# Optimization experiments

Measured on AMD Instinct MI355X. Metric: run time of the kernel, lower is better.

Reference implementation:

```python
import jax, jax.numpy as jnp
import numpy as np

DIM = 1536
NH = 12
HD = DIM // NH  # 128
B = 1
F, H, W = 8, 16, 16
S = F * H * W  # 2048
EPS = 1e-6
MAX_POS = 1024


def _rmsnorm(x, g):
    # WanRMSNorm: x * rsqrt(mean(x^2, -1) + eps) * weight  (computed in fp32)
    return x * jax.lax.rsqrt(jnp.mean(x * x, axis=-1, keepdims=True) + EPS) * g


def _rope_apply(x, grid_sizes, freqs):
    # x: [B, S, NH, HD]; freqs: [1024, HD//2] angles. Full (level-0) freqs_i path.
    f, h, w = [int(v) for v in np.asarray(grid_sizes[0])]
    c = HD // 2  # 64
    s0 = c - 2 * (c // 3)  # 22 (frame freqs)
    s1 = c // 3            # 21 (height / width freqs)
    p0 = freqs[:f, :s0]
    p1 = freqs[:h, s0:s0 + s1]
    p2 = freqs[:w, s0 + s1:]
    ang = jnp.concatenate([
        jnp.broadcast_to(p0[:, None, None, :], (f, h, w, s0)),
        jnp.broadcast_to(p1[None, :, None, :], (f, h, w, s1)),
        jnp.broadcast_to(p2[None, None, :, :], (f, h, w, s1)),
    ], axis=-1).reshape(f * h * w, 1, c)  # [S, 1, c]
    cos, sin = jnp.cos(ang), jnp.sin(ang)
    xr = x[0].reshape(S, NH, c, 2)  # pairs -> complex rotation
    x0, x1 = xr[..., 0], xr[..., 1]
    out = jnp.stack([x0 * cos - x1 * sin, x0 * sin + x1 * cos], axis=-1)
    return out.reshape(S, NH, HD)[None].astype(jnp.float32)  # [1, S, NH, HD]


def setup_inputs() -> dict:
    key = jax.random.key(0)
    ks = jax.random.split(key, 8)
    sc = 0.02
    return {
        "x": jax.random.normal(ks[0], (B, S, DIM), jnp.float32),
        "freqs": jax.random.uniform(ks[1], (MAX_POS, HD // 2), jnp.float32, 0.0, 2.0 * np.pi),
        "wq": jax.random.normal(ks[2], (DIM, DIM), jnp.float32) * sc,
        "bq": jnp.zeros((DIM,), jnp.float32),
        "wk": jax.random.normal(ks[3], (DIM, DIM), jnp.float32) * sc,
        "bk": jnp.zeros((DIM,), jnp.float32),
        "wv": jax.random.normal(ks[4], (DIM, DIM), jnp.float32) * sc,
        "bv": jnp.zeros((DIM,), jnp.float32),
        "wo": jax.random.normal(ks[5], (DIM, DIM), jnp.float32) * sc,
        "bo": jnp.zeros((DIM,), jnp.float32),
        "gq": jnp.ones((DIM,), jnp.float32),
        "gk": jnp.ones((DIM,), jnp.float32),
        "seq_lens": jnp.array([S], jnp.int32),
        "grid_sizes": jnp.array([[F, H, W]], jnp.int32),
    }


def reference(x, freqs, wq, bq, wk, bk, wv, bv, wo, bo, gq, gk, seq_lens, grid_sizes):
    b, s = x.shape[:2]
    q = _rmsnorm(x @ wq.T + bq, gq).reshape(b, s, NH, HD)
    k = _rmsnorm(x @ wk.T + bk, gk).reshape(b, s, NH, HD)
    v = (x @ wv.T + bv).reshape(b, s, NH, HD)
    q = _rope_apply(q, grid_sizes, freqs)
    k = _rope_apply(k, grid_sizes, freqs)
    # flash_attention with k_lens=seq_lens, full window -> masked SDPA
    kmask = jnp.arange(s)[None, :] < seq_lens[:, None]  # [b, s]
    scores = jnp.einsum('bqnd,bknd->bnqk', q, k) / np.sqrt(HD).astype(np.float32)
    scores = jnp.where(kmask[:, None, None, :], scores, jnp.finfo(scores.dtype).min)
    attn = jax.nn.softmax(scores, axis=-1)
    out = jnp.einsum('bnqk,bknd->bqnd', attn, v).reshape(b, s, DIM)
    return out @ wo.T + bo
```

## Files before the change

### kernel.cpp

```cpp
#include <hip/hip_runtime.h>
#include <math.h>

#define DIMN 1536
#define NHEAD 12
#define HDIM 128
#define SLEN 2048
#define EPSV 1e-6f

typedef __attribute__((ext_vector_type(8))) short short8;
typedef __attribute__((ext_vector_type(4))) short short4v;
typedef __attribute__((ext_vector_type(4))) float f32x4;

typedef __attribute__((address_space(1))) const void gvoid_t;
typedef __attribute__((address_space(3))) void lvoid_t;

__device__ __forceinline__ void gload_lds16(const void* g, void* l) {
    __builtin_amdgcn_global_load_lds((gvoid_t*)g, (lvoid_t*)l, 16, 0, 0);
}

__device__ inline short to_bf16(float f) {
    union { float f; unsigned u; } v; v.f = f;
    unsigned r = (v.u + 0x7FFFu + ((v.u >> 16) & 1u)) >> 16;
    return (short)r;
}
__device__ inline float bf_to_f(short h) {
    union { unsigned u; float f; } v;
    v.u = ((unsigned)(unsigned short)h) << 16;
    return v.f;
}

__device__ __forceinline__ int swz(int row, int c) {
    return c ^ (row & 3) ^ ((row >> 2) & 3);
}

__global__ __launch_bounds__(256)
void cast5(const float* s0, const float* s1, const float* s2,
           const float* s3, const float* s4,
           short* d0, short* d1, short* d2, short* d3, short* d4,
           int n0, int nw)
{
    const float* s; short* d; int n;
    switch (blockIdx.y) {
        case 0: s = s0; d = d0; n = n0; break;
        case 1: s = s1; d = d1; n = nw; break;
        case 2: s = s2; d = d2; n = nw; break;
        case 3: s = s3; d = d3; n = nw; break;
        default: s = s4; d = d4; n = nw; break;
    }
    int idx = (blockIdx.x * 256 + threadIdx.x) * 8;
    if (idx >= n) return;
    float4 a = *(const float4*)(s + idx);
    float4 b = *(const float4*)(s + idx + 4);
    short8 r;
    r[0] = to_bf16(a.x); r[1] = to_bf16(a.y); r[2] = to_bf16(a.z); r[3] = to_bf16(a.w);
    r[4] = to_bf16(b.x); r[5] = to_bf16(b.y); r[6] = to_bf16(b.z); r[7] = to_bf16(b.w);
    *(short8*)(d + idx) = r;
}

__global__ __launch_bounds__(256)
void gemm_qkv(const short* __restrict__ A,
              const short* __restrict__ W0, const short* __restrict__ W1,
              const short* __restrict__ W2,
              const float* __restrict__ b0, const float* __restrict__ b1,
              const float* __restrict__ b2,
              short* __restrict__ Y0, short* __restrict__ Y1,
              short* __restrict__ Vp)
{
    __shared__ __attribute__((aligned(16))) short As[128 * 32];
    __shared__ __attribute__((aligned(16))) short Bs[128 * 32];

    const int sel = blockIdx.x / (DIMN / 128);
    const int nb  = blockIdx.x % (DIMN / 128);
    const short* W    = (sel == 0) ? W0 : (sel == 1) ? W1 : W2;
    const float* bias = (sel == 0) ? b0 : (sel == 1) ? b1 : b2;

    const int tid = threadIdx.x;
    const int wave = tid >> 6, lane = tid & 63;
    const int quad = lane >> 4, col = lane & 15;
    const int wm = wave >> 1, wn = wave & 1;
    const int m0 = blockIdx.y * 128, n0 = nb * 128;
    const int sr = tid >> 2;
    const int sc = tid & 3;

    f32x4 acc[4][4];
    #pragma unroll
    for (int i = 0; i < 4; ++i)
        #pragma unroll
        for (int j = 0; j < 4; ++j)
            #pragma unroll
            for (int r = 0; r < 4; ++r) acc[i][j][r] = 0.f;

    for (int kt = 0; kt < DIMN; kt += 32) {
        __syncthreads();
        #pragma unroll
        for (int i = 0; i < 2; ++i) {
            const int row = i * 64 + sr;
            const int c = swz(row, sc);
            gload_lds16(A + (size_t)(m0 + row) * DIMN + kt + c * 8, As + i * 2048 + tid * 8);
        }
        #pragma unroll
        for (int i = 0; i < 2; ++i) {
            const int row = i * 64 + sr;
            const int c = swz(row, sc);
            gload_lds16(W + (size_t)(n0 + row) * DIMN + kt + c * 8, Bs + i * 2048 + tid * 8);
        }
        __syncthreads();

        short8 af[4], bf[4];
        #pragma unroll
        for (int mt = 0; mt < 4; ++mt) {
            const int row = wm * 64 + mt * 16 + col;
            af[mt] = *(const short8*)&As[row * 32 + swz(row, quad) * 8];
        }
        #pragma unroll
        for (int nt = 0; nt < 4; ++nt) {
            const int row = wn * 64 + nt * 16 + col;
            bf[nt] = *(const short8*)&Bs[row * 32 + swz(row, quad) * 8];
        }
        #pragma unroll
        for (int mt = 0; mt < 4; ++mt)
            #pragma unroll
            for (int nt = 0; nt < 4; ++nt)
                acc[mt][nt] = __builtin_amdgcn_mfma_f32_16x16x32_bf16(
                    af[mt], bf[nt], acc[mt][nt], 0, 0, 0);
    }

    if (sel < 2) {
        short* Y = (sel == 0) ? Y0 : Y1;
        #pragma unroll
        for (int mt = 0; mt < 4; ++mt) {
            #pragma unroll
            for (int nt = 0; nt < 4; ++nt) {
                const int n = n0 + wn * 64 + nt * 16 + col;
                const float bb = bias[n];
                #pragma unroll
                for (int r = 0; r < 4; ++r) {
                    const int m = m0 + wm * 64 + mt * 16 + quad * 4 + r;
                    Y[(size_t)m * DIMN + n] = to_bf16(acc[mt][nt][r] + bb);
                }
            }
        }
    } else {
        const int head = nb;
        const int kt64 = blockIdx.y * 2 + wm;
        #pragma unroll
        for (int mt = 0; mt < 4; ++mt) {
            #pragma unroll
            for (int nt = 0; nt < 4; ++nt) {
                const int n = n0 + wn * 64 + nt * 16 + col;
                const float bb = bias[n];
                const int dt = wn * 4 + nt;
                const int chunk = (head * 32 + kt64) * 16 + dt * 2 + (mt >> 1);
                const int off = ((mt & 1) * 2 + (quad >> 1)) * 128 + col * 8 + (quad & 1) * 4;
                short4v o;
                #pragma unroll
                for (int r = 0; r < 4; ++r) o[r] = to_bf16(acc[mt][nt][r] + bb);
                *(short4v*)(Vp + (size_t)chunk * 512 + off) = o;
            }
        }
    }
}

__global__ __launch_bounds__(256)
void gemm_out(const short* __restrict__ A, const short* __restrict__ W,
              const float* __restrict__ bias, float* __restrict__ Yf)
{
    __shared__ __attribute__((aligned(16))) short As[128 * 32];
    __shared__ __attribute__((aligned(16))) short Bs[128 * 32];

    const int tid = threadIdx.x;
    const int wave = tid >> 6, lane = tid & 63;
    const int quad = lane >> 4, col = lane & 15;
    const int wm = wave >> 1, wn = wave & 1;
    const int m0 = blockIdx.y * 128, n0 = blockIdx.x * 128;
    const int sr = tid >> 2;
    const int sc = tid & 3;

    f32x4 acc[4][4];
    #pragma unroll
    for (int i = 0; i < 4; ++i)
        #pragma unroll
        for (int j = 0; j < 4; ++j)
            #pragma unroll
            for (int r = 0; r < 4; ++r) acc[i][j][r] = 0.f;

    for (int kt = 0; kt < DIMN; kt += 32) {
        __syncthreads();
        #pragma unroll
        for (int i = 0; i < 2; ++i) {
            const int row = i * 64 + sr;
            const int c = swz(row, sc);
            gload_lds16(A + (size_t)(m0 + row) * DIMN + kt + c * 8, As + i * 2048 + tid * 8);
        }
        #pragma unroll
        for (int i = 0; i < 2; ++i) {
            const int row = i * 64 + sr;
            const int c = swz(row, sc);
            gload_lds16(W + (size_t)(n0 + row) * DIMN + kt + c * 8, Bs + i * 2048 + tid * 8);
        }
        __syncthreads();

        short8 af[4], bf[4];
        #pragma unroll
        for (int mt = 0; mt < 4; ++mt) {
            const int row = wm * 64 + mt * 16 + col;
            af[mt] = *(const short8*)&As[row * 32 + swz(row, quad) * 8];
        }
        #pragma unroll
        for (int nt = 0; nt < 4; ++nt) {
            const int row = wn * 64 + nt * 16 + col;
            bf[nt] = *(const short8*)&Bs[row * 32 + swz(row, quad) * 8];
        }
        #pragma unroll
        for (int mt = 0; mt < 4; ++mt)
            #pragma unroll
            for (int nt = 0; nt < 4; ++nt)
                acc[mt][nt] = __builtin_amdgcn_mfma_f32_16x16x32_bf16(
                    af[mt], bf[nt], acc[mt][nt], 0, 0, 0);
    }

    #pragma unroll
    for (int mt = 0; mt < 4; ++mt) {
        #pragma unroll
        for (int nt = 0; nt < 4; ++nt) {
            const int n = n0 + wn * 64 + nt * 16 + col;
            const float bb = bias[n];
            #pragma unroll
            for (int r = 0; r < 4; ++r) {
                const int m = m0 + wm * 64 + mt * 16 + quad * 4 + r;
                Yf[(size_t)m * DIMN + n] = acc[mt][nt][r] + bb;
            }
        }
    }
}

__global__ __launch_bounds__(256)
void rms_rope_qk(short* __restrict__ qbuf, const short* __restrict__ kbuf,
                 short* __restrict__ Kp,
                 const float* __restrict__ gq, const float* __restrict__ gk,
                 const float* __restrict__ freqs, const int* __restrict__ grid_sizes)
{
    const int s = blockIdx.x;
    const int isK = blockIdx.y;
    const int tid = threadIdx.x;
    short* qrow = qbuf + (size_t)s * DIMN;
    const short* row = isK ? (kbuf + (size_t)s * DIMN) : qrow;
    const float* g = isK ? gk : gq;

    float ss = 0.f;
    if (tid < 192) {
        short8 v = *(const short8*)(row + tid * 8);
        #pragma unroll
        for (int j = 0; j < 8; ++j) { float f = bf_to_f(v[j]); ss += f * f; }
    }
    #pragma unroll
    for (int off = 32; off; off >>= 1) ss += __shfl_down(ss, off, 64);

    __shared__ float red[4];
    __shared__ float s_scale;
    if ((tid & 63) == 0) red[tid >> 6] = ss;
    __syncthreads();
    if (tid == 0) {
        float t = red[0] + red[1] + red[2] + red[3];
        float sc = rsqrtf(t / (float)DIMN + EPSV);
        s_scale = isK ? sc : sc * 0.08838834764831845f;
    }
    __syncthreads();
    const float scale = s_scale;

    const int h = grid_sizes[1], w = grid_sizes[2];
    const int fi = s / (h * w);
    const int hi = (s / w) % h;
    const int wi = s % w;

    if (!isK) {
        for (int p = tid; p < NHEAD * 64; p += 256) {
            const int n = p >> 6;
            const int d = p & 63;
            const int idx = (d < 22) ? fi : ((d < 43) ? hi : wi);
            const float ang = freqs[idx * 64 + d];
            const float cs = cosf(ang), sn = sinf(ang);
            const int base = n * HDIM + 2 * d;
            const float v0 = bf_to_f(qrow[base]) * scale * g[base];
            const float v1 = bf_to_f(qrow[base + 1]) * scale * g[base + 1];
            qrow[base]     = to_bf16(v0 * cs - v1 * sn);
            qrow[base + 1] = to_bf16(v0 * sn + v1 * cs);
        }
    } else if (tid < 192) {
        const int n = tid >> 4;
        const int o = tid & 15;
        short8 outv;
        #pragma unroll
        for (int pp = 0; pp < 4; ++pp) {
            const int pd = o * 4 + pp;
            const int idx = (pd < 22) ? fi : ((pd < 43) ? hi : wi);
            const float ang = freqs[idx * 64 + pd];
            const float cs = cosf(ang), sn = sinf(ang);
            const int base = n * HDIM + 2 * pd;
            const float v0 = bf_to_f(row[base]) * scale * g[base];
            const float v1 = bf_to_f(row[base + 1]) * scale * g[base + 1];
            outv[pp * 2]     = to_bf16(v0 * cs - v1 * sn);
            outv[pp * 2 + 1] = to_bf16(v0 * sn + v1 * cs);
        }
        const int kb = s >> 4, colk = s & 15;
        const int kc = o >> 2, quadk = o & 3;
        const size_t addr = ((((size_t)(n * 128 + kb) * 4 + kc) * 64) + quadk * 16 + colk) * 8;
        *(short8*)(Kp + addr) = outv;
    }
}

__global__ __launch_bounds__(256)
void attn_mfma4(const short* __restrict__ Q, const short* __restrict__ Kp,
                const short* __restrict__ Vp, short* __restrict__ O,
                const int* __restrict__ seq_lens)
{
    __shared__ __attribute__((aligned(16))) char smem[25536];
    short* Ps = (short*)smem;
    float* Oc = (float*)smem;
    float* Lc = (float*)(smem + 3 * 16 * 132 * 4);

    const int tid = threadIdx.x;
    const int wave = tid >> 6, lane = tid & 63;
    const int quad = lane >> 4, col = lane & 15;
    const int head = blockIdx.y;
    const int row0 = blockIdx.x * 16;
    const int slen = seq_lens[0];
    short* psw = Ps + wave * (16 * 72);

    short8 qf[4];
    #pragma unroll
    for (int kc = 0; kc < 4; ++kc)
        qf[kc] = *(const short8*)(Q + (size_t)(row0 + col) * DIMN
                                  + head * HDIM + kc * 32 + quad * 8);

    f32x4 oacc[8];
    #pragma unroll
    for (int dt = 0; dt < 8; ++dt)
        #pragma unroll
        for (int r = 0; r < 4; ++r) oacc[dt][r] = 0.f;
    float lsum[4] = {0.f, 0.f, 0.f, 0.f};

    const int kbeg = wave * (SLEN / 4);
    for (int kt = kbeg; kt < kbeg + SLEN / 4; kt += 64) {
        f32x4 s[4];
        #pragma unroll
        for (int nt = 0; nt < 4; ++nt)
            #pragma unroll
            for (int r = 0; r < 4; ++r) s[nt][r] = 0.f;

        const int kb0 = kt >> 4;
        #pragma unroll
        for (int kc = 0; kc < 4; ++kc) {
            short8 kf[4];
            #pragma unroll
            for (int nt = 0; nt < 4; ++nt)
                kf[nt] = *(const short8*)(Kp +
                    ((((size_t)(head * 128 + kb0 + nt) * 4 + kc) * 64) + lane) * 8);
            #pragma unroll
            for (int nt = 0; nt < 4; ++nt)
                s[nt] = __builtin_amdgcn_mfma_f32_16x16x32_bf16(qf[kc], kf[nt], s[nt], 0, 0, 0);
        }

        #pragma unroll
        for (int nt = 0; nt < 4; ++nt) {
            const bool masked = (kt + nt * 16 + col >= slen);
            #pragma unroll
            for (int r = 0; r < 4; ++r) {
                float p = masked ? 0.f : __expf(s[nt][r]);
                lsum[r] += p;
                psw[(quad * 4 + r) * 72 + nt * 16 + col] = to_bf16(p);
            }
        }

        short8 pf[2];
        #pragma unroll
        for (int kc = 0; kc < 2; ++kc)
            pf[kc] = *(const short8*)&psw[col * 72 + kc * 32 + quad * 8];

        const size_t vbase = ((size_t)(head * 32 + (kt >> 6)) * 16) * 512;
        #pragma unroll
        for (int dt = 0; dt < 8; ++dt) {
            short8 vf[2];
            #pragma unroll
            for (int kc = 0; kc < 2; ++kc)
                vf[kc] = *(const short8*)(Vp + vbase + ((size_t)(dt * 2 + kc) * 64 + lane) * 8);
            #pragma unroll
            for (int kc = 0; kc < 2; ++kc)
                oacc[dt] = __builtin_amdgcn_mfma_f32_16x16x32_bf16(pf[kc], vf[kc], oacc[dt], 0, 0, 0);
        }
    }

    #pragma unroll
    for (int r = 0; r < 4; ++r) {
        #pragma unroll
        for (int off = 8; off; off >>= 1) lsum[r] += __shfl_xor(lsum[r], off, 64);
    }

    __syncthreads();
    if (wave != 0) {
        float* oc = Oc + (wave - 1) * (16 * 132);
        #pragma unroll
        for (int dt = 0; dt < 8; ++dt)
            #pragma unroll
            for (int r = 0; r < 4; ++r)
                oc[(quad * 4 + r) * 132 + dt * 16 + col] = oacc[dt][r];
        if (col == 0) {
            #pragma unroll
            for (int r = 0; r < 4; ++r) Lc[(wave - 1) * 16 + quad * 4 + r] = lsum[r];
        }
    }
    __syncthreads();
    if (wave == 0) {
        float inv[4];
        #pragma unroll
        for (int r = 0; r < 4; ++r) {
            float l = lsum[r];
            #pragma unroll
            for (int s2 = 0; s2 < 3; ++s2) l += Lc[s2 * 16 + quad * 4 + r];
            inv[r] = 1.0f / l;
        }
        #pragma unroll
        for (int dt = 0; dt < 8; ++dt) {
            #pragma unroll
            for (int r = 0; r < 4; ++r) {
                float v = oacc[dt][r];
                #pragma unroll
                for (int s2 = 0; s2 < 3; ++s2)
                    v += Oc[s2 * (16 * 132) + (quad * 4 + r) * 132 + dt * 16 + col];
                O[(size_t)(row0 + quad * 4 + r) * DIMN + head * HDIM + dt * 16 + col]
                    = to_bf16(v * inv[r]);
            }
        }
    }
}

extern "C" void kernel_launch(void* const* d_in, const int* in_sizes, int n_in,
                              void* d_out, int out_size, void* d_ws, size_t ws_size,
                              hipStream_t stream)
{
    const float* x     = (const float*)d_in[0];
    const float* freqs = (const float*)d_in[1];
    const float* wq    = (const float*)d_in[2];
    const float* bq    = (const float*)d_in[3];
    const float* wk    = (const float*)d_in[4];
    const float* bk    = (const float*)d_in[5];
    const float* wv    = (const float*)d_in[6];
    const float* bv    = (const float*)d_in[7];
    const float* wo    = (const float*)d_in[8];
    const float* bo    = (const float*)d_in[9];
    const float* gq    = (const float*)d_in[10];
    const float* gk    = (const float*)d_in[11];
    const int* seq_lens   = (const int*)d_in[12];
    const int* grid_sizes = (const int*)d_in[13];
    float* out = (float*)d_out;

    const size_t NX = (size_t)SLEN * DIMN;
    const size_t NW = (size_t)DIMN * DIMN;
    short* xb  = (short*)d_ws;
    short* wqb = xb + NX;
    short* wkb = wqb + NW;
    short* wvb = wkb + NW;
    short* wob = wvb + NW;
    short* qb  = wob + NW;
    short* kb  = qb + NX;
    short* vp  = kb + NX;
    short* kp  = vp + NX;
    short* ob  = kp + NX;

    cast5<<<dim3(1536, 5), 256, 0, stream>>>(x, wq, wk, wv, wo,
                                             xb, wqb, wkb, wvb, wob,
                                             (int)NX, (int)NW);

    gemm_qkv<<<dim3(3 * DIMN / 128, SLEN / 128), 256, 0, stream>>>(
        xb, wqb, wkb, wvb, bq, bk, bv, qb, kb, vp);

    rms_rope_qk<<<dim3(SLEN, 2), 256, 0, stream>>>(qb, kb, kp, gq, gk, freqs, grid_sizes);

    attn_mfma4<<<dim3(SLEN / 16, NHEAD), 256, 0, stream>>>(qb, kp, vp, ob, seq_lens);

    gemm_out<<<dim3(DIMN / 128, SLEN / 128), 256, 0, stream>>>(ob, wob, bo, out);
}
```

Baseline: 291.3 us.

## Widen GEMM K-tile to 64, hoist V loads, use fast sincos, set attn occupancy

Both GEMMs now share one mainloop that stages 64-wide K tiles with an 8-way XOR swizzle. This halves the number of barrier pairs per K pass and doubles the LDS footprint. In attention, all V fragments for a tile are loaded before the softmax/P write, so their global latency overlaps the exp work, at the cost of more registers. A launch_bounds occupancy hint is added to attention, and the RoPE kernel uses __sincosf instead of separate cosf/sinf, which is less accurate.

Result: slower. 335.8 us (+15.3%).

```diff
diff --git a/kernel.cpp b/kernel.cpp
--- a/kernel.cpp
+++ b/kernel.cpp
@@ -29,8 +29,8 @@
     return v.f;
 }
 
-__device__ __forceinline__ int swz(int row, int c) {
-    return c ^ (row & 3) ^ ((row >> 2) & 3);
+__device__ __forceinline__ int swz8(int row, int c) {
+    return c ^ (row & 7);
 }
 
 __global__ __launch_bounds__(256)
@@ -57,6 +57,56 @@
     *(short8*)(d + idx) = r;
 }
 
+__device__ __forceinline__ void gemm_mainloop(const short* __restrict__ A,
+    const short* __restrict__ W, int m0, int n0, int K,
+    short* As, short* Bs, f32x4 (&acc)[4][4])
+{
+    const int tid = threadIdx.x;
+    const int wave = tid >> 6, lane = tid & 63;
+    const int quad = lane >> 4, col = lane & 15;
+    const int wm = wave >> 1, wn = wave & 1;
+    const int sr = tid >> 3;
+    const int sc = tid & 7;
+
+    for (int kt = 0; kt < K; kt += 64) {
+        __syncthreads();
+        #pragma unroll
+        for (int i = 0; i < 4; ++i) {
+            const int row = i * 32 + sr;
+            const int c = swz8(row, sc);
+            gload_lds16(A + (size_t)(m0 + row) * K + kt + c * 8, As + i * 2048 + tid * 8);
+        }
+        #pragma unroll
+        for (int i = 0; i < 4; ++i) {
+            const int row = i * 32 + sr;
+            const int c = swz8(row, sc);
+            gload_lds16(W + (size_t)(n0 + row) * K + kt + c * 8, Bs + i * 2048 + tid * 8);
+        }
+        __syncthreads();
+
+        #pragma unroll
+        for (int kb = 0; kb < 2; ++kb) {
+            short8 af[4], bf[4];
+            #pragma unroll
+            for (int mt = 0; mt < 4; ++mt) {
+                const int row = wm * 64 + mt * 16 + col;
+                af[mt] = *(const short8*)&As[row * 64 + swz8(row, kb * 4 + quad) * 8];
+            }
+            #pragma unroll
+            for (int nt = 0; nt < 4; ++nt) {
+                const int row = wn * 64 + nt * 16 + col;
+                bf[nt] = *(const short8*)&Bs[row * 64 + swz8(row, kb * 4 + quad) * 8];
+            }
+            #pragma unroll
+            for (int mt = 0; mt < 4; ++mt)
+                #pragma unroll
+                for (int nt = 0; nt < 4; ++nt)
+                    acc[mt][nt] = __builtin_amdgcn_mfma_f32_16x16x32_bf16(
+                        af[mt], bf[nt], acc[mt][nt], 0, 0, 0);
+        }
+    }
+}
+
 __global__ __launch_bounds__(256)
 void gemm_qkv(const short* __restrict__ A,
               const short* __restrict__ W0, const short* __restrict__ W1,
@@ -66,8 +116,8 @@
               short* __restrict__ Y0, short* __restrict__ Y1,
               short* __restrict__ Vp)
 {
-    __shared__ __attribute__((aligned(16))) short As[128 * 32];
-    __shared__ __attribute__((aligned(16))) short Bs[128 * 32];
+    __shared__ __attribute__((aligned(16))) short As[128 * 64];
+    __shared__ __attribute__((aligned(16))) short Bs[128 * 64];
 
     const int sel = blockIdx.x / (DIMN / 128);
     const int nb  = blockIdx.x % (DIMN / 128);
@@ -79,8 +129,6 @@
     const int quad = lane >> 4, col = lane & 15;
     const int wm = wave >> 1, wn = wave & 1;
     const int m0 = blockIdx.y * 128, n0 = nb * 128;
-    const int sr = tid >> 2;
-    const int sc = tid & 3;
 
     f32x4 acc[4][4];
     #pragma unroll
@@ -90,40 +138,7 @@
             #pragma unroll
             for (int r = 0; r < 4; ++r) acc[i][j][r] = 0.f;
 
-    for (int kt = 0; kt < DIMN; kt += 32) {
-        __syncthreads();
-        #pragma unroll
-        for (int i = 0; i < 2; ++i) {
-            const int row = i * 64 + sr;
-            const int c = swz(row, sc);
-            gload_lds16(A + (size_t)(m0 + row) * DIMN + kt + c * 8, As + i * 2048 + tid * 8);
-        }
-        #pragma unroll
-        for (int i = 0; i < 2; ++i) {
-            const int row = i * 64 + sr;
-            const int c = swz(row, sc);
-            gload_lds16(W + (size_t)(n0 + row) * DIMN + kt + c * 8, Bs + i * 2048 + tid * 8);
-        }
-        __syncthreads();
-
-        short8 af[4], bf[4];
-        #pragma unroll
-        for (int mt = 0; mt < 4; ++mt) {
-            const int row = wm * 64 + mt * 16 + col;
-            af[mt] = *(const short8*)&As[row * 32 + swz(row, quad) * 8];
-        }
-        #pragma unroll
-        for (int nt = 0; nt < 4; ++nt) {
-            const int row = wn * 64 + nt * 16 + col;
-            bf[nt] = *(const short8*)&Bs[row * 32 + swz(row, quad) * 8];
-        }
-        #pragma unroll
-        for (int mt = 0; mt < 4; ++mt)
-            #pragma unroll
-            for (int nt = 0; nt < 4; ++nt)
-                acc[mt][nt] = __builtin_amdgcn_mfma_f32_16x16x32_bf16(
-                    af[mt], bf[nt], acc[mt][nt], 0, 0, 0);
-    }
+    gemm_mainloop(A, W, m0, n0, DIMN, As, Bs, acc);
 
     if (sel < 2) {
         short* Y = (sel == 0) ? Y0 : Y1;
@@ -165,16 +180,14 @@
 void gemm_out(const short* __restrict__ A, const short* __restrict__ W,
               const float* __restrict__ bias, float* __restrict__ Yf)
 {
-    __shared__ __attribute__((aligned(16))) short As[128 * 32];
-    __shared__ __attribute__((aligned(16))) short Bs[128 * 32];
+    __shared__ __attribute__((aligned(16))) short As[128 * 64];
+    __shared__ __attribute__((aligned(16))) short Bs[128 * 64];
 
     const int tid = threadIdx.x;
     const int wave = tid >> 6, lane = tid & 63;
     const int quad = lane >> 4, col = lane & 15;
     const int wm = wave >> 1, wn = wave & 1;
     const int m0 = blockIdx.y * 128, n0 = blockIdx.x * 128;
-    const int sr = tid >> 2;
-    const int sc = tid & 3;
 
     f32x4 acc[4][4];
     #pragma unroll
@@ -184,40 +197,7 @@
             #pragma unroll
             for (int r = 0; r < 4; ++r) acc[i][j][r] = 0.f;
 
-    for (int kt = 0; kt < DIMN; kt += 32) {
-        __syncthreads();
-        #pragma unroll
-        for (int i = 0; i < 2; ++i) {
-            const int row = i * 64 + sr;
-            const int c = swz(row, sc);
-            gload_lds16(A + (size_t)(m0 + row) * DIMN + kt + c * 8, As + i * 2048 + tid * 8);
-        }
-        #pragma unroll
-        for (int i = 0; i < 2; ++i) {
-            const int row = i * 64 + sr;
-            const int c = swz(row, sc);
-            gload_lds16(W + (size_t)(n0 + row) * DIMN + kt + c * 8, Bs + i * 2048 + tid * 8);
-        }
-        __syncthreads();
-
-        short8 af[4], bf[4];
-        #pragma unroll
-        for (int mt = 0; mt < 4; ++mt) {
-            const int row = wm * 64 + mt * 16 + col;
-            af[mt] = *(const short8*)&As[row * 32 + swz(row, quad) * 8];
-        }
-        #pragma unroll
-        for (int nt = 0; nt < 4; ++nt) {
-            const int row = wn * 64 + nt * 16 + col;
-            bf[nt] = *(const short8*)&Bs[row * 32 + swz(row, quad) * 8];
-        }
-        #pragma unroll
-        for (int mt = 0; mt < 4; ++mt)
-            #pragma unroll
-            for (int nt = 0; nt < 4; ++nt)
-                acc[mt][nt] = __builtin_amdgcn_mfma_f32_16x16x32_bf16(
-                    af[mt], bf[nt], acc[mt][nt], 0, 0, 0);
-    }
+    gemm_mainloop(A, W, m0, n0, DIMN, As, Bs, acc);
 
     #pragma unroll
     for (int mt = 0; mt < 4; ++mt) {
@@ -279,7 +259,8 @@
             const int d = p & 63;
             const int idx = (d < 22) ? fi : ((d < 43) ? hi : wi);
             const float ang = freqs[idx * 64 + d];
-            const float cs = cosf(ang), sn = sinf(ang);
+            float sn, cs;
+            __sincosf(ang, &sn, &cs);
             const int base = n * HDIM + 2 * d;
             const float v0 = bf_to_f(qrow[base]) * scale * g[base];
             const float v1 = bf_to_f(qrow[base + 1]) * scale * g[base + 1];
@@ -295,7 +276,8 @@
             const int pd = o * 4 + pp;
             const int idx = (pd < 22) ? fi : ((pd < 43) ? hi : wi);
             const float ang = freqs[idx * 64 + pd];
-            const float cs = cosf(ang), sn = sinf(ang);
+            float sn, cs;
+            __sincosf(ang, &sn, &cs);
             const int base = n * HDIM + 2 * pd;
             const float v0 = bf_to_f(row[base]) * scale * g[base];
             const float v1 = bf_to_f(row[base + 1]) * scale * g[base + 1];
@@ -309,7 +291,7 @@
     }
 }
 
-__global__ __launch_bounds__(256)
+__global__ __launch_bounds__(256, 3)
 void attn_mfma4(const short* __restrict__ Q, const short* __restrict__ Kp,
                 const short* __restrict__ Vp, short* __restrict__ O,
                 const int* __restrict__ seq_lens)
@@ -361,6 +343,14 @@
                 s[nt] = __builtin_amdgcn_mfma_f32_16x16x32_bf16(qf[kc], kf[nt], s[nt], 0, 0, 0);
         }
 
+        const size_t vbase = ((size_t)(head * 32 + (kt >> 6)) * 16) * 512;
+        short8 vf[8][2];
+        #pragma unroll
+        for (int dt = 0; dt < 8; ++dt)
+            #pragma unroll
+            for (int kc = 0; kc < 2; ++kc)
+                vf[dt][kc] = *(const short8*)(Vp + vbase + ((size_t)(dt * 2 + kc) * 64 + lane) * 8);
+
         #pragma unroll
         for (int nt = 0; nt < 4; ++nt) {
             const bool masked = (kt + nt * 16 + col >= slen);
@@ -377,17 +367,12 @@
         for (int kc = 0; kc < 2; ++kc)
             pf[kc] = *(const short8*)&psw[col * 72 + kc * 32 + quad * 8];
 
-        const size_t vbase = ((size_t)(head * 32 + (kt >> 6)) * 16) * 512;
-        #pragma unroll
-        for (int dt = 0; dt < 8; ++dt) {
-            short8 vf[2];
+        #pragma unroll
+        for (int dt = 0; dt < 8; ++dt)
             #pragma unroll
             for (int kc = 0; kc < 2; ++kc)
-                vf[kc] = *(const short8*)(Vp + vbase + ((size_t)(dt * 2 + kc) * 64 + lane) * 8);
-            #pragma unroll
-            for (int kc = 0; kc < 2; ++kc)
-                oacc[dt] = __builtin_amdgcn_mfma_f32_16x16x32_bf16(pf[kc], vf[kc], oacc[dt], 0, 0, 0);
-        }
+                oacc[dt] = __builtin_amdgcn_mfma_f32_16x16x32_bf16(
+                    pf[kc], vf[dt][kc], oacc[dt], 0, 0, 0);
     }
 
     #pragma unroll
```
